# Kernel optimization log

Measured on AMD Instinct MI355X. Metric: run time of the kernel, lower is better.

The kernel has to match this reference:

```python
import jax, jax.numpy as jnp
import numpy as np

B, T, N_EMBD, HEAD_SIZE = 8, 2048, 1024, 128

def setup_inputs() -> dict:
    key = jax.random.key(0)
    kx, kk, kq, kv = jax.random.split(key, 4)
    scale = 1.0 / np.sqrt(N_EMBD)
    return {
        "x": jax.random.normal(kx, (B, T, N_EMBD), dtype=jnp.float32),
        "Wk": jax.random.normal(kk, (N_EMBD, HEAD_SIZE), dtype=jnp.float32) * scale,
        "Wq": jax.random.normal(kq, (N_EMBD, HEAD_SIZE), dtype=jnp.float32) * scale,
        "Wv": jax.random.normal(kv, (N_EMBD, HEAD_SIZE), dtype=jnp.float32) * scale,
    }

def reference(x, Wk, Wq, Wv):
    # x: [B, T, C]; projections: [C, H]
    k = jnp.einsum("btc,ch->bth", x, Wk)
    q = jnp.einsum("btc,ch->bth", x, Wq)
    v = jnp.einsum("btc,ch->bth", x, Wv)
    # NOTE: original code does tf.divide(scores, 1/sqrt(n_embd)) == scores * sqrt(n_embd)
    wei = jnp.einsum("bqh,bkh->bqk", q, k) * jnp.sqrt(jnp.float32(N_EMBD))  # [B, T, T]
    # causal mask via band_part (zero out upper triangle) then zeros -> -inf, as in source
    tril = jnp.tril(wei)
    wei = jnp.where(tril == 0.0, -jnp.inf, tril)
    wei = jax.nn.softmax(wei, axis=-1)
    out = jnp.einsum("bqk,bkh->bqh", wei, v)  # [B, T, H]
    return out
```

## Files before the change

kernel.cpp:

```cpp
#include <hip/hip_runtime.h>
#include <hip/hip_bf16.h>

typedef float  f32x4  __attribute__((ext_vector_type(4)));
typedef __bf16 bf16x8 __attribute__((ext_vector_type(8)));
typedef unsigned int   u32;
typedef unsigned short u16;
typedef u32   u32x2  __attribute__((ext_vector_type(2)));
typedef u32   u32x4  __attribute__((ext_vector_type(4)));
typedef u16   u16x4  __attribute__((ext_vector_type(4)));
typedef u16   u16x8  __attribute__((ext_vector_type(8)));

#define DEV __device__ __forceinline__

constexpr int NB = 8, T = 2048, C = 1024, H = 128;
constexpr int BT = NB * T;

union Frag {
  bf16x8 v;
  u32x4  u4;
  u32x2  u2[2];
  u32    u[4];
  u16    s[8];
};

DEV u16 f2bu(float f) {
  __hip_bfloat16 h = __float2bfloat16(f);
  return __builtin_bit_cast(u16, h);
}
DEV float bu2f(u16 u) {
  return __bfloat162float(__builtin_bit_cast(__hip_bfloat16, u));
}
DEV f32x4 MFMA(bf16x8 a, bf16x8 b, f32x4 c) {
  return __builtin_amdgcn_mfma_f32_16x16x32_bf16(a, b, c, 0, 0, 0);
}


__global__ void prep_w(const float* __restrict__ Wk, const float* __restrict__ Wq,
                       const float* __restrict__ Wv,
                       u16* __restrict__ wpq, u16* __restrict__ wpk,
                       u16* __restrict__ wpv) {
  const int id = blockIdx.x * 256 + threadIdx.x;
  if (id >= 24 * 32 * 64) return;
  const int lane = id & 63;
  const int kc   = (id >> 6) & 31;
  const int tile = id >> 11;
  const int mat  = tile >> 3;
  const int tt   = tile & 7;
  const int n    = tt * 16 + (lane & 15);
  const float* W = (mat == 0) ? Wq : (mat == 1) ? Wk : Wv;
  u16x8 hi, lo;
  #pragma unroll
  for (int e = 0; e < 8; ++e) {
    const int k = kc * 32 + 4 * (lane >> 4) + (e & 3) + 16 * (e >> 2);
    const float w = W[(size_t)k * H + n];
    u16 h = f2bu(w);
    hi[e] = h;
    lo[e] = f2bu(w - bu2f(h));
  }
  if (mat == 2) {
    *(u16x8*)(wpv + ((size_t)(tt * 32 + kc) * 64 + lane) * 8) = hi;
  } else {
    u16* p = ((mat == 0) ? wpq : wpk) +
             (((size_t)(tt * 32 + kc) * 2 + 0) * 64 + lane) * 8;
    *(u16x8*)p         = hi;
    *(u16x8*)(p + 512) = lo;
  }
}

__global__ __launch_bounds__(1024, 4) void proj_kernel(
    const float* __restrict__ x,
    const u16* __restrict__ wpq, const u16* __restrict__ wpk,
    const u16* __restrict__ wpv,
    u16* __restrict__ qpk, u16* __restrict__ kpk, u16* __restrict__ vpk) {
  __shared__ u16 xh[64][72];
  __shared__ u16 xl[64][72];
  const int tid  = threadIdx.x;
  const int m0   = blockIdx.x * 64;
  const int w    = tid >> 6;
  const int lane = tid & 63;
  const int lg   = lane >> 4, lc = lane & 15;
  const int wrow = (w & 3) * 16;
  const int nq   = w >> 2;

  f32x4 zero = {0.f, 0.f, 0.f, 0.f};
  f32x4 acc[6];
  #pragma unroll
  for (int i = 0; i < 6; ++i) acc[i] = zero;

  const int lrow = tid >> 4;
  const int lcol = (tid & 15) * 4;

  for (int ks = 0; ks < 16; ++ks) {
    const f32x4 xv = *(const f32x4*)&x[(size_t)(m0 + lrow) * C + ks * 64 + lcol];
    u16x4 hv, lv;
    #pragma unroll
    for (int e = 0; e < 4; ++e) {
      u16 h = f2bu(xv[e]);
      hv[e] = h;
      lv[e] = f2bu(xv[e] - bu2f(h));
    }
    __syncthreads();
    *(u16x4*)&xh[lrow][lcol] = hv;
    *(u16x4*)&xl[lrow][lcol] = lv;
    __syncthreads();

    #pragma unroll
    for (int kc = 0; kc < 2; ++kc) {
      Frag axh, axl;
      axh.u2[0] = *(const u32x2*)&xh[wrow + lc][kc * 32 + 4 * lg];
      axh.u2[1] = *(const u32x2*)&xh[wrow + lc][kc * 32 + 16 + 4 * lg];
      axl.u2[0] = *(const u32x2*)&xl[wrow + lc][kc * 32 + 4 * lg];
      axl.u2[1] = *(const u32x2*)&xl[wrow + lc][kc * 32 + 16 + 4 * lg];
      const int kcg = ks * 2 + kc;

      #pragma unroll
      for (int i = 0; i < 6; ++i) {
        const int tn = nq + 4 * i;
        const int mat = tn >> 3, tt = tn & 7;
        if (mat < 2) {
          const u16* pw = ((mat == 0) ? wpq : wpk) +
                          ((size_t)(tt * 32 + kcg) * 2 * 64 + lane) * 8;
          Frag bh, bl;
          bh.u4 = *(const u32x4*)pw;
          bl.u4 = *(const u32x4*)(pw + 512);
          acc[i] = MFMA(axh.v, bh.v, acc[i]);
          acc[i] = MFMA(axh.v, bl.v, acc[i]);
          acc[i] = MFMA(axl.v, bh.v, acc[i]);
        } else {
          Frag bh;
          bh.u4 = *(const u32x4*)(wpv + ((size_t)(tt * 32 + kcg) * 64 + lane) * 8);
          acc[i] = MFMA(axh.v, bh.v, acc[i]);
        }
      }
    }
  }

  const int tb_abs = (m0 + wrow) >> 4;
  const int b  = tb_abs >> 7;
  const int tb = tb_abs & 127;
  #pragma unroll
  for (int i = 0; i < 6; ++i) {
    const int tn = nq + 4 * i;
    const int mat = tn >> 3, tt = tn & 7;
    #pragma unroll
    for (int r = 0; r < 4; ++r) {
      const float val = acc[i][r];
      if (mat < 2) {
        const u16 hvv = f2bu(val);
        const u16 lvv = f2bu(val - bu2f(hvv));
        const int lane_c = 4 * lg + r + 16 * (lc >> 2);
        const int hs = tt >> 1;
        const int e  = (lc & 3) + 4 * (tt & 1);
        u16* dst = ((mat == 0) ? qpk : kpk) +
                   (((size_t)(b * 128 + tb) * 4 + hs) * 2 * 64 + lane_c) * 8 + e;
        dst[0]   = hvv;
        dst[512] = lvv;
      } else {
        const int kt = tb >> 1;
        const int lane_c = lc + 16 * lg;
        const int e = r + 4 * (tb & 1);
        vpk[(((size_t)(b * 64 + kt) * 8 + tt) * 64 + lane_c) * 8 + e] = f2bu(val);
      }
    }
  }
}

__global__ __launch_bounds__(512, 4) void attn_kernel(
    const u16* __restrict__ qpk, const u16* __restrict__ kpk,
    const u16* __restrict__ vpk, float* __restrict__ out) {
  __shared__ float lm[8][16];
  __shared__ float ll[8][16];
  __shared__ u16 lo[8][16][132];

  const int bid = blockIdx.x;
  const int b   = bid & 7;
  const int qt  = bid >> 3;
  const int w    = threadIdx.x >> 6;
  const int lane = threadIdx.x & 63;
  const int lg = lane >> 4, lc = lane & 15;

  Frag bqh[4], bql[4];
  const u16* qp = qpk + (size_t)(b * 128 + qt) * 4096 + lane * 8;
  #pragma unroll
  for (int hs = 0; hs < 4; ++hs) {
    bqh[hs].u4 = *(const u32x4*)(qp + (size_t)(hs * 2 + 0) * 512);
    bql[hs].u4 = *(const u32x4*)(qp + (size_t)(hs * 2 + 1) * 512);
  }

  f32x4 zero = {0.f, 0.f, 0.f, 0.f};
  f32x4 o_acc[8];
  #pragma unroll
  for (int i = 0; i < 8; ++i) o_acc[i] = zero;
  float m_run = -INFINITY, l_run = 0.f;

  const int myq = qt * 16 + lc;
  const int nkb = qt >> 2;

  for (int kb = w; kb <= nkb; kb += 8) {
    f32x4 s[4];
    #pragma unroll
    for (int t = 0; t < 4; ++t) s[t] = zero;

    const u16* kp = kpk + (size_t)(b * 128 + kb * 4) * 4096 + lane * 8;
    #pragma unroll
    for (int t = 0; t < 4; ++t) {
      #pragma unroll
      for (int hs = 0; hs < 4; ++hs) {
        const u16* p = kp + (size_t)(t * 8 + hs * 2) * 512;
        Frag akh, akl;
        akh.u4 = *(const u32x4*)p;
        akl.u4 = *(const u32x4*)(p + 512);
        s[t] = MFMA(akh.v, bqh[hs].v, s[t]);
        s[t] = MFMA(akh.v, bql[hs].v, s[t]);
        s[t] = MFMA(akl.v, bqh[hs].v, s[t]);
      }
    }

    float pmax = -INFINITY;
    #pragma unroll
    for (int t = 0; t < 4; ++t) {
      #pragma unroll
      for (int r = 0; r < 4; ++r) {
        const int kk = kb * 64 + t * 16 + 4 * lg + r;
        float v = s[t][r] * 32.0f;
        if (kk > myq || v == 0.0f) v = -INFINITY;
        s[t][r] = v;
        pmax = fmaxf(pmax, v);
      }
    }
    pmax = fmaxf(pmax, __shfl_xor(pmax, 16));
    pmax = fmaxf(pmax, __shfl_xor(pmax, 32));
    const float m_new = fmaxf(m_run, pmax);
    const float alpha = __expf(m_run - m_new);

    float sum = 0.f;
    u16 pb[16];
    #pragma unroll
    for (int t = 0; t < 4; ++t) {
      #pragma unroll
      for (int r = 0; r < 4; ++r) {
        const float p = __expf(s[t][r] - m_new);
        sum += p;
        pb[t * 4 + r] = f2bu(p);
      }
    }
    sum += __shfl_xor(sum, 16);
    sum += __shfl_xor(sum, 32);
    l_run = l_run * alpha + sum;
    m_run = m_new;

    float al[4];
    #pragma unroll
    for (int r = 0; r < 4; ++r) al[r] = __shfl(alpha, 4 * lg + r);
    #pragma unroll
    for (int i = 0; i < 8; ++i) {
      #pragma unroll
      for (int r = 0; r < 4; ++r) o_acc[i][r] *= al[r];
    }

    Frag pa[2];
    #pragma unroll
    for (int ks = 0; ks < 2; ++ks) {
      #pragma unroll
      for (int e = 0; e < 8; ++e)
        pa[ks].s[e] = pb[(2 * ks + (e >> 2)) * 4 + (e & 3)];
    }

    #pragma unroll
    for (int ks = 0; ks < 2; ++ks) {
      const u16* vp = vpk + (size_t)(b * 64 + kb * 2 + ks) * 4096 + lane * 8;
      #pragma unroll
      for (int ht = 0; ht < 8; ++ht) {
        Frag bv;
        bv.u4 = *(const u32x4*)(vp + (size_t)ht * 512);
        o_acc[ht] = MFMA(pa[ks].v, bv.v, o_acc[ht]);
      }
    }
  }

  if (lane < 16) { lm[w][lane] = m_run; ll[w][lane] = l_run; }
  #pragma unroll
  for (int ht = 0; ht < 8; ++ht)
    #pragma unroll
    for (int r = 0; r < 4; ++r)
      lo[w][4 * lg + r][ht * 16 + lc] = f2bu(o_acc[ht][r]);
  __syncthreads();

  const int tid = threadIdx.x;
  const int q  = tid >> 5;
  const int hb = (tid & 31) * 4;
  float M = -INFINITY;
  #pragma unroll
  for (int ww = 0; ww < 8; ++ww) M = fmaxf(M, lm[ww][q]);
  float lsum = 0.f;
  f32x4 osum = {0.f, 0.f, 0.f, 0.f};
  #pragma unroll
  for (int ww = 0; ww < 8; ++ww) {
    const float sc = __expf(lm[ww][q] - M);
    lsum += sc * ll[ww][q];
    const u16x4 ov = *(const u16x4*)&lo[ww][q][hb];
    #pragma unroll
    for (int j = 0; j < 4; ++j) osum[j] += sc * bu2f(ov[j]);
  }
  const float inv = 1.0f / lsum;
  f32x4 res = {osum[0] * inv, osum[1] * inv, osum[2] * inv, osum[3] * inv};
  *(f32x4*)&out[((size_t)(b * T + qt * 16 + q)) * H + hb] = res;
}

extern "C" void kernel_launch(void* const* d_in, const int* in_sizes, int n_in,
                              void* d_out, int out_size, void* d_ws, size_t ws_size,
                              hipStream_t stream) {
  (void)in_sizes; (void)n_in; (void)out_size; (void)ws_size;
  const float* x  = (const float*)d_in[0];
  const float* Wk = (const float*)d_in[1];
  const float* Wq = (const float*)d_in[2];
  const float* Wv = (const float*)d_in[3];
  float* out = (float*)d_out;

  u16* w = (u16*)d_ws;
  const size_t WPQK = (size_t)8 * 32 * 2 * 64 * 8;
  const size_t WPV  = (size_t)8 * 32 * 64 * 8;
  const size_t QKP  = (size_t)NB * 128 * 4 * 2 * 64 * 8;
  const size_t VP   = (size_t)NB * 64 * 8 * 64 * 8;
  u16* wpq = w;
  u16* wpk = wpq + WPQK;
  u16* wpv = wpk + WPQK;
  u16* qpk = wpv + WPV;
  u16* kpk = qpk + QKP;
  u16* vpk = kpk + QKP;

  prep_w<<<192, 256, 0, stream>>>(Wk, Wq, Wv, wpq, wpk, wpv);
  proj_kernel<<<BT / 64, 1024, 0, stream>>>(x, wpq, wpk, wpv, qpk, kpk, vpk);
  attn_kernel<<<NB * (T / 16), 512, 0, stream>>>(qpk, kpk, vpk, out);
}
```

Baseline: 118.8 us.

## Split projection by output column groups and process two query tiles per attention block

The projection kernel now uses 256-thread blocks, each covering a 64-row tile for one column group of Q/K/V, giving 1024 smaller blocks instead of 256 large ones. The attention kernel now handles 32 queries per block (two 16-row tiles), so each K and V fragment load feeds two sets of MFMAs. This halves K/V global traffic per query and doubles the work per load. In exchange it raises register pressure (launch bounds drop to 2 blocks), and the projection kernel now reloads x once per column group, four times in total.

```diff
diff --git a/kernel.cpp b/kernel.cpp
--- a/kernel.cpp
+++ b/kernel.cpp
@@ -67,7 +67,7 @@
   }
 }
 
-__global__ __launch_bounds__(1024, 4) void proj_kernel(
+__global__ __launch_bounds__(256, 8) void proj_kernel(
     const float* __restrict__ x,
     const u16* __restrict__ wpq, const u16* __restrict__ wpk,
     const u16* __restrict__ wpv,
@@ -75,33 +75,43 @@
   __shared__ u16 xh[64][72];
   __shared__ u16 xl[64][72];
   const int tid  = threadIdx.x;
-  const int m0   = blockIdx.x * 64;
+  const int ng   = blockIdx.x >> 8;
+  const int mt   = blockIdx.x & 255;
+  const int m0   = mt * 64;
   const int w    = tid >> 6;
   const int lane = tid & 63;
   const int lg   = lane >> 4, lc = lane & 15;
-  const int wrow = (w & 3) * 16;
-  const int nq   = w >> 2;
+  const int wrow = w * 16;
 
   f32x4 zero = {0.f, 0.f, 0.f, 0.f};
   f32x4 acc[6];
   #pragma unroll
   for (int i = 0; i < 6; ++i) acc[i] = zero;
 
-  const int lrow = tid >> 4;
-  const int lcol = (tid & 15) * 4;
+  const int lrow = tid >> 2;
+  const int lcs  = (tid & 3) * 16;
 
   for (int ks = 0; ks < 16; ++ks) {
-    const f32x4 xv = *(const f32x4*)&x[(size_t)(m0 + lrow) * C + ks * 64 + lcol];
-    u16x4 hv, lv;
-    #pragma unroll
-    for (int e = 0; e < 4; ++e) {
-      u16 h = f2bu(xv[e]);
-      hv[e] = h;
-      lv[e] = f2bu(xv[e] - bu2f(h));
+    f32x4 xv[4];
+    #pragma unroll
+    for (int j = 0; j < 4; ++j)
+      xv[j] = *(const f32x4*)&x[(size_t)(m0 + lrow) * C + ks * 64 + lcs + 4 * j];
+    u16x4 hv[4], lv[4];
+    #pragma unroll
+    for (int j = 0; j < 4; ++j) {
+      #pragma unroll
+      for (int e = 0; e < 4; ++e) {
+        u16 h = f2bu(xv[j][e]);
+        hv[j][e] = h;
+        lv[j][e] = f2bu(xv[j][e] - bu2f(h));
+      }
     }
     __syncthreads();
-    *(u16x4*)&xh[lrow][lcol] = hv;
-    *(u16x4*)&xl[lrow][lcol] = lv;
+    #pragma unroll
+    for (int j = 0; j < 4; ++j) {
+      *(u16x4*)&xh[lrow][lcs + 4 * j] = hv[j];
+      *(u16x4*)&xl[lrow][lcs + 4 * j] = lv[j];
+    }
     __syncthreads();
 
     #pragma unroll
@@ -114,37 +124,37 @@
       const int kcg = ks * 2 + kc;
 
       #pragma unroll
-      for (int i = 0; i < 6; ++i) {
-        const int tn = nq + 4 * i;
-        const int mat = tn >> 3, tt = tn & 7;
+      for (int j = 0; j < 6; ++j) {
+        const int mat = j >> 1;
+        const int tt  = 2 * ng + (j & 1);
         if (mat < 2) {
           const u16* pw = ((mat == 0) ? wpq : wpk) +
-                          ((size_t)(tt * 32 + kcg) * 2 * 64 + lane) * 8;
+                          (size_t)(tt * 32 + kcg) * 1024 + lane * 8;
           Frag bh, bl;
           bh.u4 = *(const u32x4*)pw;
           bl.u4 = *(const u32x4*)(pw + 512);
-          acc[i] = MFMA(axh.v, bh.v, acc[i]);
-          acc[i] = MFMA(axh.v, bl.v, acc[i]);
-          acc[i] = MFMA(axl.v, bh.v, acc[i]);
+          acc[j] = MFMA(axh.v, bh.v, acc[j]);
+          acc[j] = MFMA(axh.v, bl.v, acc[j]);
+          acc[j] = MFMA(axl.v, bh.v, acc[j]);
         } else {
           Frag bh;
-          bh.u4 = *(const u32x4*)(wpv + ((size_t)(tt * 32 + kcg) * 64 + lane) * 8);
-          acc[i] = MFMA(axh.v, bh.v, acc[i]);
+          bh.u4 = *(const u32x4*)(wpv + (size_t)(tt * 32 + kcg) * 512 + lane * 8);
+          acc[j] = MFMA(axh.v, bh.v, acc[j]);
         }
       }
     }
   }
 
-  const int tb_abs = (m0 + wrow) >> 4;
+  const int tb_abs = mt * 4 + w;
   const int b  = tb_abs >> 7;
   const int tb = tb_abs & 127;
   #pragma unroll
-  for (int i = 0; i < 6; ++i) {
-    const int tn = nq + 4 * i;
-    const int mat = tn >> 3, tt = tn & 7;
+  for (int j = 0; j < 6; ++j) {
+    const int mat = j >> 1;
+    const int tt  = 2 * ng + (j & 1);
     #pragma unroll
     for (int r = 0; r < 4; ++r) {
-      const float val = acc[i][r];
+      const float val = acc[j][r];
       if (mat < 2) {
         const u16 hvv = f2bu(val);
         const u16 lvv = f2bu(val - bu2f(hvv));
@@ -165,41 +175,47 @@
   }
 }
 
-__global__ __launch_bounds__(512, 4) void attn_kernel(
+__global__ __launch_bounds__(512, 2) void attn_kernel(
     const u16* __restrict__ qpk, const u16* __restrict__ kpk,
     const u16* __restrict__ vpk, float* __restrict__ out) {
-  __shared__ float lm[8][16];
-  __shared__ float ll[8][16];
-  __shared__ u16 lo[8][16][132];
+  __shared__ float lm[8][32];
+  __shared__ float ll[8][32];
+  __shared__ u16 lo[8][32][132];
 
   const int bid = blockIdx.x;
   const int b   = bid & 7;
-  const int qt  = bid >> 3;
+  const int qp  = bid >> 3;
   const int w    = threadIdx.x >> 6;
   const int lane = threadIdx.x & 63;
   const int lg = lane >> 4, lc = lane & 15;
 
-  Frag bqh[4], bql[4];
-  const u16* qp = qpk + (size_t)(b * 128 + qt) * 4096 + lane * 8;
-  #pragma unroll
-  for (int hs = 0; hs < 4; ++hs) {
-    bqh[hs].u4 = *(const u32x4*)(qp + (size_t)(hs * 2 + 0) * 512);
-    bql[hs].u4 = *(const u32x4*)(qp + (size_t)(hs * 2 + 1) * 512);
-  }
+  Frag bqh[2][4], bql[2][4];
+  const u16* qb = qpk + (size_t)(b * 128 + 2 * qp) * 4096 + lane * 8;
+  #pragma unroll
+  for (int tq = 0; tq < 2; ++tq)
+    #pragma unroll
+    for (int hs = 0; hs < 4; ++hs) {
+      bqh[tq][hs].u4 = *(const u32x4*)(qb + tq * 4096 + (size_t)(hs * 2 + 0) * 512);
+      bql[tq][hs].u4 = *(const u32x4*)(qb + tq * 4096 + (size_t)(hs * 2 + 1) * 512);
+    }
 
   f32x4 zero = {0.f, 0.f, 0.f, 0.f};
-  f32x4 o_acc[8];
-  #pragma unroll
-  for (int i = 0; i < 8; ++i) o_acc[i] = zero;
-  float m_run = -INFINITY, l_run = 0.f;
-
-  const int myq = qt * 16 + lc;
-  const int nkb = qt >> 2;
+  f32x4 o_acc[2][8];
+  #pragma unroll
+  for (int tq = 0; tq < 2; ++tq)
+    #pragma unroll
+    for (int i = 0; i < 8; ++i) o_acc[tq][i] = zero;
+  float m_run[2] = {-INFINITY, -INFINITY};
+  float l_run[2] = {0.f, 0.f};
+
+  const int nkb = qp >> 1;
 
   for (int kb = w; kb <= nkb; kb += 8) {
-    f32x4 s[4];
-    #pragma unroll
-    for (int t = 0; t < 4; ++t) s[t] = zero;
+    f32x4 s[2][4];
+    #pragma unroll
+    for (int tq = 0; tq < 2; ++tq)
+      #pragma unroll
+      for (int t = 0; t < 4; ++t) s[tq][t] = zero;
 
     const u16* kp = kpk + (size_t)(b * 128 + kb * 4) * 4096 + lane * 8;
     #pragma unroll
@@ -210,60 +226,65 @@
         Frag akh, akl;
         akh.u4 = *(const u32x4*)p;
         akl.u4 = *(const u32x4*)(p + 512);
-        s[t] = MFMA(akh.v, bqh[hs].v, s[t]);
-        s[t] = MFMA(akh.v, bql[hs].v, s[t]);
-        s[t] = MFMA(akl.v, bqh[hs].v, s[t]);
-      }
-    }
-
-    float pmax = -INFINITY;
-    #pragma unroll
-    for (int t = 0; t < 4; ++t) {
-      #pragma unroll
-      for (int r = 0; r < 4; ++r) {
-        const int kk = kb * 64 + t * 16 + 4 * lg + r;
-        float v = s[t][r] * 32.0f;
-        if (kk > myq || v == 0.0f) v = -INFINITY;
-        s[t][r] = v;
-        pmax = fmaxf(pmax, v);
-      }
-    }
-    pmax = fmaxf(pmax, __shfl_xor(pmax, 16));
-    pmax = fmaxf(pmax, __shfl_xor(pmax, 32));
-    const float m_new = fmaxf(m_run, pmax);
-    const float alpha = __expf(m_run - m_new);
-
-    float sum = 0.f;
-    u16 pb[16];
-    #pragma unroll
-    for (int t = 0; t < 4; ++t) {
-      #pragma unroll
-      for (int r = 0; r < 4; ++r) {
-        const float p = __expf(s[t][r] - m_new);
-        sum += p;
-        pb[t * 4 + r] = f2bu(p);
-      }
-    }
-    sum += __shfl_xor(sum, 16);
-    sum += __shfl_xor(sum, 32);
-    l_run = l_run * alpha + sum;
-    m_run = m_new;
-
-    float al[4];
-    #pragma unroll
-    for (int r = 0; r < 4; ++r) al[r] = __shfl(alpha, 4 * lg + r);
-    #pragma unroll
-    for (int i = 0; i < 8; ++i) {
-      #pragma unroll
-      for (int r = 0; r < 4; ++r) o_acc[i][r] *= al[r];
-    }
-
-    Frag pa[2];
-    #pragma unroll
-    for (int ks = 0; ks < 2; ++ks) {
-      #pragma unroll
-      for (int e = 0; e < 8; ++e)
-        pa[ks].s[e] = pb[(2 * ks + (e >> 2)) * 4 + (e & 3)];
+        s[0][t] = MFMA(akh.v, bqh[0][hs].v, s[0][t]);
+        s[0][t] = MFMA(akh.v, bql[0][hs].v, s[0][t]);
+        s[0][t] = MFMA(akl.v, bqh[0][hs].v, s[0][t]);
+        s[1][t] = MFMA(akh.v, bqh[1][hs].v, s[1][t]);
+        s[1][t] = MFMA(akh.v, bql[1][hs].v, s[1][t]);
+        s[1][t] = MFMA(akl.v, bqh[1][hs].v, s[1][t]);
+      }
+    }
+
+    Frag pa[2][2];
+    #pragma unroll
+    for (int tq = 0; tq < 2; ++tq) {
+      const int myq = 32 * qp + 16 * tq + lc;
+      float pmax = -INFINITY;
+      #pragma unroll
+      for (int t = 0; t < 4; ++t) {
+        #pragma unroll
+        for (int r = 0; r < 4; ++r) {
+          const int kk = kb * 64 + t * 16 + 4 * lg + r;
+          float v = s[tq][t][r] * 32.0f;
+          if (kk > myq || v == 0.0f) v = -INFINITY;
+          s[tq][t][r] = v;
+          pmax = fmaxf(pmax, v);
+        }
+      }
+      pmax = fmaxf(pmax, __shfl_xor(pmax, 16));
+      pmax = fmaxf(pmax, __shfl_xor(pmax, 32));
+      const float m_new = fmaxf(m_run[tq], pmax);
+      const float alpha = __expf(m_run[tq] - m_new);
+
+      float sum = 0.f;
+      u16 pb[16];
+      #pragma unroll
+      for (int t = 0; t < 4; ++t) {
+        #pragma unroll
+        for (int r = 0; r < 4; ++r) {
+          const float p = __expf(s[tq][t][r] - m_new);
+          sum += p;
+          pb[t * 4 + r] = f2bu(p);
+        }
+      }
+      sum += __shfl_xor(sum, 16);
+      sum += __shfl_xor(sum, 32);
+      l_run[tq] = l_run[tq] * alpha + sum;
+      m_run[tq] = m_new;
+
+      float al[4];
+      #pragma unroll
+      for (int r = 0; r < 4; ++r) al[r] = __shfl(alpha, 4 * lg + r);
+      #pragma unroll
+      for (int i = 0; i < 8; ++i) {
+        #pragma unroll
+        for (int r = 0; r < 4; ++r) o_acc[tq][i][r] *= al[r];
+      }
+      #pragma unroll
+      for (int ks = 0; ks < 2; ++ks)
+        #pragma unroll
+        for (int e = 0; e < 8; ++e)
+          pa[tq][ks].s[e] = pb[(2 * ks + (e >> 2)) * 4 + (e & 3)];
     }
 
     #pragma unroll
@@ -273,38 +294,50 @@
       for (int ht = 0; ht < 8; ++ht) {
         Frag bv;
         bv.u4 = *(const u32x4*)(vp + (size_t)ht * 512);
-        o_acc[ht] = MFMA(pa[ks].v, bv.v, o_acc[ht]);
-      }
-    }
-  }
-
-  if (lane < 16) { lm[w][lane] = m_run; ll[w][lane] = l_run; }
-  #pragma unroll
-  for (int ht = 0; ht < 8; ++ht)
-    #pragma unroll
-    for (int r = 0; r < 4; ++r)
-      lo[w][4 * lg + r][ht * 16 + lc] = f2bu(o_acc[ht][r]);
+        o_acc[0][ht] = MFMA(pa[0][ks].v, bv.v, o_acc[0][ht]);
+        o_acc[1][ht] = MFMA(pa[1][ks].v, bv.v, o_acc[1][ht]);
+      }
+    }
+  }
+
+  if (lane < 16) {
+    lm[w][lane]      = m_run[0];
+    lm[w][16 + lane] = m_run[1];
+    ll[w][lane]      = l_run[0];
+    ll[w][16 + lane] = l_run[1];
+  }
+  #pragma unroll
+  for (int tq = 0; tq < 2; ++tq)
+    #pragma unroll
+    for (int ht = 0; ht < 8; ++ht)
+      #pragma unroll
+      for (int r = 0; r < 4; ++r)
+        lo[w][16 * tq + 4 * lg + r][ht * 16 + lc] = f2bu(o_acc[tq][ht][r]);
   __syncthreads();
 
   const int tid = threadIdx.x;
-  const int q  = tid >> 5;
-  const int hb = (tid & 31) * 4;
-  float M = -INFINITY;
-  #pragma unroll
-  for (int ww = 0; ww < 8; ++ww) M = fmaxf(M, lm[ww][q]);
-  float lsum = 0.f;
-  f32x4 osum = {0.f, 0.f, 0.f, 0.f};
-  #pragma unroll
-  for (int ww = 0; ww < 8; ++ww) {
-    const float sc = __expf(lm[ww][q] - M);
-    lsum += sc * ll[ww][q];
-    const u16x4 ov = *(const u16x4*)&lo[ww][q][hb];
-    #pragma unroll
-    for (int j = 0; j < 4; ++j) osum[j] += sc * bu2f(ov[j]);
-  }
-  const float inv = 1.0f / lsum;
-  f32x4 res = {osum[0] * inv, osum[1] * inv, osum[2] * inv, osum[3] * inv};
-  *(f32x4*)&out[((size_t)(b * T + qt * 16 + q)) * H + hb] = res;
+  #pragma unroll
+  for (int it = 0; it < 2; ++it) {
+    const int item = tid + it * 512;
+    const int q  = item >> 5;
+    const int hb = (item & 31) * 4;
+    float M = -INFINITY;
+    #pragma unroll
+    for (int ww = 0; ww < 8; ++ww) M = fmaxf(M, lm[ww][q]);
+    float lsum = 0.f;
+    f32x4 osum = {0.f, 0.f, 0.f, 0.f};
+    #pragma unroll
+    for (int ww = 0; ww < 8; ++ww) {
+      const float sc = __expf(lm[ww][q] - M);
+      lsum += sc * ll[ww][q];
+      const u16x4 ov = *(const u16x4*)&lo[ww][q][hb];
+      #pragma unroll
+      for (int j = 0; j < 4; ++j) osum[j] += sc * bu2f(ov[j]);
+    }
+    const float inv = 1.0f / lsum;
+    f32x4 res = {osum[0] * inv, osum[1] * inv, osum[2] * inv, osum[3] * inv};
+    *(f32x4*)&out[((size_t)(b * T + 32 * qp + q)) * H + hb] = res;
+  }
 }
 
 extern "C" void kernel_launch(void* const* d_in, const int* in_sizes, int n_in,
@@ -321,7 +354,6 @@
   const size_t WPQK = (size_t)8 * 32 * 2 * 64 * 8;
   const size_t WPV  = (size_t)8 * 32 * 64 * 8;
   const size_t QKP  = (size_t)NB * 128 * 4 * 2 * 64 * 8;
-  const size_t VP   = (size_t)NB * 64 * 8 * 64 * 8;
   u16* wpq = w;
   u16* wpk = wpq + WPQK;
   u16* wpv = wpk + WPQK;
@@ -330,6 +362,6 @@
   u16* vpk = kpk + QKP;
 
   prep_w<<<192, 256, 0, stream>>>(Wk, Wq, Wv, wpq, wpk, wpv);
-  proj_kernel<<<BT / 64, 1024, 0, stream>>>(x, wpq, wpk, wpv, qpk, kpk, vpk);
-  attn_kernel<<<NB * (T / 16), 512, 0, stream>>>(qpk, kpk, vpk, out);
-}
+  proj_kernel<<<1024, 256, 0, stream>>>(x, wpq, wpk, wpv, qpk, kpk, vpk);
+  attn_kernel<<<512, 512, 0, stream>>>(qpk, kpk, vpk, out);
+}
```

New measurement: 146.8 us. +23.6%, slower.

## Retile projection GEMM into 128-row by column-group blocks with LDS-staged weights

Applied to the files above, without the earlier changes.

The projection kernel now uses 256-thread blocks covering 128 rows of x and one of four column groups (two 16-wide tiles each of Q, K and V). Each block stages that group's weight fragments in shared memory instead of every wave reading them from global memory. Each wave computes two row sub-tiles so every weight fragment feeds twice as many MFMAs. The trade-off is that x is now loaded and split into hi/lo four times, once per column group, instead of once, and the grid grows to 512 blocks.

```diff
diff --git a/kernel.cpp b/kernel.cpp
--- a/kernel.cpp
+++ b/kernel.cpp
@@ -67,99 +67,156 @@
   }
 }
 
-__global__ __launch_bounds__(1024, 4) void proj_kernel(
+__global__ __launch_bounds__(256, 4) void proj_kernel(
     const float* __restrict__ x,
     const u16* __restrict__ wpq, const u16* __restrict__ wpk,
     const u16* __restrict__ wpv,
     u16* __restrict__ qpk, u16* __restrict__ kpk, u16* __restrict__ vpk) {
-  __shared__ u16 xh[64][72];
-  __shared__ u16 xl[64][72];
+  __shared__ u16 xh[128][72];
+  __shared__ u16 xl[128][72];
+  __shared__ u16 wsl[2 * 10 * 64 * 8];
   const int tid  = threadIdx.x;
-  const int m0   = blockIdx.x * 64;
+  const int ng   = blockIdx.x >> 7;
+  const int mt   = blockIdx.x & 127;
+  const int m0   = mt * 128;
   const int w    = tid >> 6;
   const int lane = tid & 63;
   const int lg   = lane >> 4, lc = lane & 15;
-  const int wrow = (w & 3) * 16;
-  const int nq   = w >> 2;
 
   f32x4 zero = {0.f, 0.f, 0.f, 0.f};
-  f32x4 acc[6];
-  #pragma unroll
-  for (int i = 0; i < 6; ++i) acc[i] = zero;
-
-  const int lrow = tid >> 4;
-  const int lcol = (tid & 15) * 4;
+  f32x4 acc[6][2];
+  #pragma unroll
+  for (int j = 0; j < 6; ++j)
+    #pragma unroll
+    for (int s = 0; s < 2; ++s) acc[j][s] = zero;
+
+  const int lrow  = tid >> 1;
+  const int lcs32 = (tid & 1) * 32;
 
   for (int ks = 0; ks < 16; ++ks) {
-    const f32x4 xv = *(const f32x4*)&x[(size_t)(m0 + lrow) * C + ks * 64 + lcol];
-    u16x4 hv, lv;
-    #pragma unroll
-    for (int e = 0; e < 4; ++e) {
-      u16 h = f2bu(xv[e]);
-      hv[e] = h;
-      lv[e] = f2bu(xv[e] - bu2f(h));
-    }
+    f32x4 xv[8];
+    #pragma unroll
+    for (int j = 0; j < 8; ++j)
+      xv[j] = *(const f32x4*)&x[(size_t)(m0 + lrow) * C + ks * 64 + lcs32 + 4 * j];
+
+    u16x8 wreg[5];
+    #pragma unroll
+    for (int i = 0; i < 5; ++i) {
+      const int c = tid + 256 * i;
+      const int kcg   = c >= 640;
+      const int rem   = c - kcg * 640;
+      const int plane = rem >> 6;
+      const int ln    = rem & 63;
+      const int kabs  = ks * 2 + kcg;
+      const u16* src;
+      if (plane < 4)
+        src = wpq + (size_t)((2 * ng + (plane >> 1)) * 32 + kabs) * 1024 +
+              (plane & 1) * 512 + ln * 8;
+      else if (plane < 8)
+        src = wpk + (size_t)((2 * ng + ((plane - 4) >> 1)) * 32 + kabs) * 1024 +
+              ((plane - 4) & 1) * 512 + ln * 8;
+      else
+        src = wpv + (size_t)((2 * ng + (plane - 8)) * 32 + kabs) * 512 + ln * 8;
+      wreg[i] = *(const u16x8*)src;
+    }
+
+    u16x4 hv[8], lv[8];
+    #pragma unroll
+    for (int j = 0; j < 8; ++j) {
+      #pragma unroll
+      for (int e = 0; e < 4; ++e) {
+        u16 h = f2bu(xv[j][e]);
+        hv[j][e] = h;
+        lv[j][e] = f2bu(xv[j][e] - bu2f(h));
+      }
+    }
+
     __syncthreads();
-    *(u16x4*)&xh[lrow][lcol] = hv;
-    *(u16x4*)&xl[lrow][lcol] = lv;
+    #pragma unroll
+    for (int j = 0; j < 8; ++j) {
+      *(u16x4*)&xh[lrow][lcs32 + 4 * j] = hv[j];
+      *(u16x4*)&xl[lrow][lcs32 + 4 * j] = lv[j];
+    }
+    #pragma unroll
+    for (int i = 0; i < 5; ++i)
+      *(u16x8*)&wsl[(size_t)(tid + 256 * i) * 8] = wreg[i];
     __syncthreads();
 
     #pragma unroll
     for (int kc = 0; kc < 2; ++kc) {
-      Frag axh, axl;
-      axh.u2[0] = *(const u32x2*)&xh[wrow + lc][kc * 32 + 4 * lg];
-      axh.u2[1] = *(const u32x2*)&xh[wrow + lc][kc * 32 + 16 + 4 * lg];
-      axl.u2[0] = *(const u32x2*)&xl[wrow + lc][kc * 32 + 4 * lg];
-      axl.u2[1] = *(const u32x2*)&xl[wrow + lc][kc * 32 + 16 + 4 * lg];
-      const int kcg = ks * 2 + kc;
-
-      #pragma unroll
-      for (int i = 0; i < 6; ++i) {
-        const int tn = nq + 4 * i;
-        const int mat = tn >> 3, tt = tn & 7;
+      Frag axh[2], axl[2];
+      #pragma unroll
+      for (int s = 0; s < 2; ++s) {
+        const int row = 32 * w + 16 * s + lc;
+        axh[s].u2[0] = *(const u32x2*)&xh[row][kc * 32 + 4 * lg];
+        axh[s].u2[1] = *(const u32x2*)&xh[row][kc * 32 + 16 + 4 * lg];
+        axl[s].u2[0] = *(const u32x2*)&xl[row][kc * 32 + 4 * lg];
+        axl[s].u2[1] = *(const u32x2*)&xl[row][kc * 32 + 16 + 4 * lg];
+      }
+      #pragma unroll
+      for (int jt = 0; jt < 2; ++jt) {
+        {
+          Frag bh, bl;
+          bh.u4 = *(const u32x4*)&wsl[((size_t)(kc * 10 + jt * 2 + 0) * 64 + lane) * 8];
+          bl.u4 = *(const u32x4*)&wsl[((size_t)(kc * 10 + jt * 2 + 1) * 64 + lane) * 8];
+          #pragma unroll
+          for (int s = 0; s < 2; ++s) {
+            acc[jt][s] = MFMA(axh[s].v, bh.v, acc[jt][s]);
+            acc[jt][s] = MFMA(axh[s].v, bl.v, acc[jt][s]);
+            acc[jt][s] = MFMA(axl[s].v, bh.v, acc[jt][s]);
+          }
+        }
+        {
+          Frag bh, bl;
+          bh.u4 = *(const u32x4*)&wsl[((size_t)(kc * 10 + 4 + jt * 2 + 0) * 64 + lane) * 8];
+          bl.u4 = *(const u32x4*)&wsl[((size_t)(kc * 10 + 4 + jt * 2 + 1) * 64 + lane) * 8];
+          #pragma unroll
+          for (int s = 0; s < 2; ++s) {
+            acc[2 + jt][s] = MFMA(axh[s].v, bh.v, acc[2 + jt][s]);
+            acc[2 + jt][s] = MFMA(axh[s].v, bl.v, acc[2 + jt][s]);
+            acc[2 + jt][s] = MFMA(axl[s].v, bh.v, acc[2 + jt][s]);
+          }
+        }
+        {
+          Frag bh;
+          bh.u4 = *(const u32x4*)&wsl[((size_t)(kc * 10 + 8 + jt) * 64 + lane) * 8];
+          #pragma unroll
+          for (int s = 0; s < 2; ++s)
+            acc[4 + jt][s] = MFMA(axh[s].v, bh.v, acc[4 + jt][s]);
+        }
+      }
+    }
+  }
+
+  #pragma unroll
+  for (int s = 0; s < 2; ++s) {
+    const int tb_abs = mt * 8 + 2 * w + s;
+    const int b  = tb_abs >> 7;
+    const int tb = tb_abs & 127;
+    #pragma unroll
+    for (int j = 0; j < 6; ++j) {
+      const int mat = j >> 1;
+      const int jt  = j & 1;
+      const int tt  = 2 * ng + jt;
+      #pragma unroll
+      for (int r = 0; r < 4; ++r) {
+        const float val = acc[j][s][r];
         if (mat < 2) {
-          const u16* pw = ((mat == 0) ? wpq : wpk) +
-                          ((size_t)(tt * 32 + kcg) * 2 * 64 + lane) * 8;
-          Frag bh, bl;
-          bh.u4 = *(const u32x4*)pw;
-          bl.u4 = *(const u32x4*)(pw + 512);
-          acc[i] = MFMA(axh.v, bh.v, acc[i]);
-          acc[i] = MFMA(axh.v, bl.v, acc[i]);
-          acc[i] = MFMA(axl.v, bh.v, acc[i]);
+          const u16 hvv = f2bu(val);
+          const u16 lvv = f2bu(val - bu2f(hvv));
+          const int lane_c = 4 * lg + r + 16 * (lc >> 2);
+          const int hs = tt >> 1;
+          const int e  = (lc & 3) + 4 * (tt & 1);
+          u16* dst = ((mat == 0) ? qpk : kpk) +
+                     (((size_t)(b * 128 + tb) * 4 + hs) * 2 * 64 + lane_c) * 8 + e;
+          dst[0]   = hvv;
+          dst[512] = lvv;
         } else {
-          Frag bh;
-          bh.u4 = *(const u32x4*)(wpv + ((size_t)(tt * 32 + kcg) * 64 + lane) * 8);
-          acc[i] = MFMA(axh.v, bh.v, acc[i]);
+          const int kt = tb >> 1;
+          const int lane_c = lc + 16 * lg;
+          const int e = r + 4 * (tb & 1);
+          vpk[(((size_t)(b * 64 + kt) * 8 + tt) * 64 + lane_c) * 8 + e] = f2bu(val);
         }
-      }
-    }
-  }
-
-  const int tb_abs = (m0 + wrow) >> 4;
-  const int b  = tb_abs >> 7;
-  const int tb = tb_abs & 127;
-  #pragma unroll
-  for (int i = 0; i < 6; ++i) {
-    const int tn = nq + 4 * i;
-    const int mat = tn >> 3, tt = tn & 7;
-    #pragma unroll
-    for (int r = 0; r < 4; ++r) {
-      const float val = acc[i][r];
-      if (mat < 2) {
-        const u16 hvv = f2bu(val);
-        const u16 lvv = f2bu(val - bu2f(hvv));
-        const int lane_c = 4 * lg + r + 16 * (lc >> 2);
-        const int hs = tt >> 1;
-        const int e  = (lc & 3) + 4 * (tt & 1);
-        u16* dst = ((mat == 0) ? qpk : kpk) +
-                   (((size_t)(b * 128 + tb) * 4 + hs) * 2 * 64 + lane_c) * 8 + e;
-        dst[0]   = hvv;
-        dst[512] = lvv;
-      } else {
-        const int kt = tb >> 1;
-        const int lane_c = lc + 16 * lg;
-        const int e = r + 4 * (tb & 1);
-        vpk[(((size_t)(b * 64 + kt) * 8 + tt) * 64 + lane_c) * 8 + e] = f2bu(val);
       }
     }
   }
@@ -321,7 +378,6 @@
   const size_t WPQK = (size_t)8 * 32 * 2 * 64 * 8;
   const size_t WPV  = (size_t)8 * 32 * 64 * 8;
   const size_t QKP  = (size_t)NB * 128 * 4 * 2 * 64 * 8;
-  const size_t VP   = (size_t)NB * 64 * 8 * 64 * 8;
   u16* wpq = w;
   u16* wpk = wpq + WPQK;
   u16* wpv = wpk + WPQK;
@@ -330,6 +386,6 @@
   u16* vpk = kpk + QKP;
 
   prep_w<<<192, 256, 0, stream>>>(Wk, Wq, Wv, wpq, wpk, wpv);
-  proj_kernel<<<BT / 64, 1024, 0, stream>>>(x, wpq, wpk, wpv, qpk, kpk, vpk);
+  proj_kernel<<<512, 256, 0, stream>>>(x, wpq, wpk, wpv, qpk, kpk, vpk);
   attn_kernel<<<NB * (T / 16), 512, 0, stream>>>(qpk, kpk, vpk, out);
 }
```

Result: faster. 112.0 us (-5.7%).
